# Optimization experiments

Measured on AMD Instinct MI355X. Metric: run time of the kernel, lower is better.

The kernel has to match this reference:

```python
import jax, jax.numpy as jnp
import numpy as np

N_QUBITS = 12
N_LAYERS = 5
OUTPUT_DIM = 4
BATCH = 1024


def _apply_1q(state, U, q, n):
    # state: (B, 2^n) complex; U: (B, 2, 2) per-sample unitary on wire q
    B = state.shape[0]
    s = state.reshape(B, 2 ** q, 2, -1)
    s = jnp.einsum('bik,bakc->baic', U, s)
    return s.reshape(B, -1)


def _cnot(state, c, t, n):
    # CNOT with control wire c, target wire t (wire 0 = most significant bit)
    B = state.shape[0]
    s = state.reshape((B,) + (2,) * n)
    s0 = jax.lax.index_in_dim(s, 0, axis=1 + c, keepdims=True)
    s1 = jax.lax.index_in_dim(s, 1, axis=1 + c, keepdims=True)
    s1 = jnp.flip(s1, axis=1 + t)  # X on target where control = 1
    return jnp.concatenate([s0, s1], axis=1 + c).reshape(B, -1)


def _forward(x, input_weights, theta, output_weights):
    n, L, D = N_QUBITS, N_LAYERS, OUTPUT_DIM
    x = jnp.tanh(x)
    B = x.shape[0]
    # |0...0> initial state, batched
    state = jnp.zeros((B, 2 ** n), jnp.complex64).at[:, 0].set(1.0)
    for l in range(L):
        # data re-uploading: RX(input_weights[l,j] * x[:,j]) on every wire, every layer
        a = input_weights[l][None, :] * x          # (B, n) RX angles
        b = theta[l, :, 0]                          # (n,) RY angles
        c = theta[l, :, 1]                          # (n,) RZ angles
        ca = jnp.cos(a / 2).astype(jnp.complex64)
        sa = jnp.sin(a / 2).astype(jnp.complex64)
        Rx = jnp.stack([jnp.stack([ca, -1j * sa], -1),
                        jnp.stack([-1j * sa, ca], -1)], -2)  # (B, n, 2, 2)
        cb = jnp.cos(b / 2).astype(jnp.complex64)
        sb = jnp.sin(b / 2).astype(jnp.complex64)
        ec = jnp.exp(-1j * c.astype(jnp.complex64) / 2)      # e^{-i c/2}
        # M = RZ(c) @ RY(b), shared across the batch
        M = jnp.stack([jnp.stack([ec * cb, -ec * sb], -1),
                       jnp.stack([jnp.conj(ec) * sb, jnp.conj(ec) * cb], -1)], -2)  # (n,2,2)
        # fused single-qubit unitary U = RZ @ RY @ RX per (sample, wire)
        U = jnp.einsum('qik,bqkj->bqij', M, Rx)
        for q in range(n):
            state = _apply_1q(state, U[:, q], q, n)
        for i in range(n):
            state = _cnot(state, i, (i + 1) % n, n)
    # exact <Z_i> on the first D wires
    p = jnp.abs(state) ** 2  # (B, 2^n)
    zs = []
    for i in range(D):
        pr = p.reshape(B, 2 ** i, 2, -1)
        zs.append(pr[:, :, 0, :].sum((1, 2)) - pr[:, :, 1, :].sum((1, 2)))
    Q = jnp.stack(zs, axis=1)  # (B, D)
    return output_weights[None, :] * Q


def setup_inputs() -> dict:
    key = jax.random.key(0)
    k1, k2, k3, k4 = jax.random.split(key, 4)
    return {
        'x': jax.random.normal(k1, (BATCH, N_QUBITS), jnp.float32),
        'input_weights': jax.random.normal(k2, (N_LAYERS, N_QUBITS), jnp.float32),
        'theta': jax.random.normal(k3, (N_LAYERS, N_QUBITS, 2), jnp.float32),
        'output_weights': jax.random.normal(k4, (OUTPUT_DIM,), jnp.float32),
    }


def reference(x, input_weights, theta, output_weights):
    return _forward(x, input_weights, theta, output_weights)
```

## Files before the change

### kernel.cpp

```cpp
#include <hip/hip_runtime.h>

#define NQ 12
#define NL 5
#define TPB 256

__host__ __device__ constexpr int sfx12_(int x) {
    x ^= x >> 1; x ^= x >> 2; x ^= x >> 4; x ^= x >> 8;
    return x & 0xFFF;
}
__host__ __device__ constexpr int par_(int x) {
    int y = x; y ^= y >> 8; y ^= y >> 4; y ^= y >> 2; y ^= y >> 1;
    return y & 1;
}
__host__ __device__ constexpr int amp_addr(int i) {
    const int g = i >> 1;
    const int G = g ^ ((g >> 3) & 7);
    return (G << 4) | ((i & 1) << 3);
}
__host__ __device__ constexpr int scat_c(int m) {
    const int s = sfx12_(m << 8);
    return amp_addr(s ^ ((s & 1) << 11));
}
__host__ __device__ constexpr int bpat(int m) { return amp_addr(m << 4); }
__host__ __device__ constexpr int meas_h(int m) {
    const int d = sfx12_(m << 8) ^ (par_(m) << 11);
    return (d >> 8) & 15;
}

__device__ __forceinline__ void gate_pair(float2 &a, float2 &c,
        const float2 u00, const float2 u01, const float2 u10, const float2 u11) {
    float2 n0, n1;
    n0.x = fmaf(u00.x, a.x, fmaf(-u00.y, a.y, fmaf(u01.x, c.x, -u01.y * c.y)));
    n0.y = fmaf(u00.x, a.y, fmaf( u00.y, a.x, fmaf(u01.x, c.y,  u01.y * c.x)));
    n1.x = fmaf(u10.x, a.x, fmaf(-u10.y, a.y, fmaf(u11.x, c.x, -u11.y * c.y)));
    n1.y = fmaf(u10.x, a.y, fmaf( u10.y, a.x, fmaf(u11.x, c.y,  u11.y * c.x)));
    a = n0; c = n1;
}
template <int K>
__device__ __forceinline__ void apply_gate(float2 (&v)[16], const float2* __restrict__ Uq) {
    const float2 u00 = Uq[0], u01 = Uq[1], u10 = Uq[2], u11 = Uq[3];
#pragma unroll
    for (int h = 0; h < 8; ++h) {
        const int m0 = ((h >> K) << (K + 1)) | (h & ((1 << K) - 1));
        gate_pair(v[m0], v[m0 | (1 << K)], u00, u01, u10, u11);
    }
}

extern "C" __global__ void __launch_bounds__(TPB)
qnet_kernel(const float* __restrict__ x, const float* __restrict__ iw,
            const float* __restrict__ th, const float* __restrict__ ow,
            float* __restrict__ out) {
    __shared__ float2 st[4096];
    __shared__ __align__(16) float2 U[NL][NQ][4];
    __shared__ float wz[4][4];
    char* stb = (char*)st;

    const int b = blockIdx.x;
    const int tid = threadIdx.x;
    const int w = tid >> 6;

    if (tid < NL * NQ) {
        const int l = tid / NQ, q = tid % NQ;
        const float xv = tanhf(x[b * NQ + q]);
        const float a = iw[l * NQ + q] * xv;
        const float bt = th[(l * NQ + q) * 2 + 0];
        const float ct = th[(l * NQ + q) * 2 + 1];
        float sa, ca; sincosf(0.5f * a, &sa, &ca);
        float sb, cb; sincosf(0.5f * bt, &sb, &cb);
        float sc, cc; sincosf(0.5f * ct, &sc, &cc);
        const float M00r = cc * cb, M00i = -sc * cb;
        const float M01r = -cc * sb, M01i = sc * sb;
        const float M10r = cc * sb, M10i = sc * sb;
        const float M11r = cc * cb, M11i = sc * cb;
        U[l][q][0] = make_float2(fmaf(M00r, ca,  sa * M01i), fmaf(M00i, ca, -sa * M01r));
        U[l][q][1] = make_float2(fmaf(ca, M01r,  sa * M00i), fmaf(ca, M01i, -sa * M00r));
        U[l][q][2] = make_float2(fmaf(M10r, ca,  sa * M11i), fmaf(M10i, ca, -sa * M11r));
        U[l][q][3] = make_float2(fmaf(ca, M11r,  sa * M10i), fmaf(ca, M11i, -sa * M10r));
    }

    const int baseA = amp_addr(tid << 4);
    const int baseB = amp_addr(((tid >> 4) << 8) | (tid & 15));
    const int baseC = amp_addr(tid);
    const int pt = __popc(tid) & 1;
    const int baseS = amp_addr(sfx12_(tid) ^ (pt << 11));
    const int hT = pt << 3;

    __syncthreads();

    float2 v[16];
#pragma unroll 1
    for (int l = 0; l < NL; ++l) {
        if (l == 0) {
#pragma unroll
            for (int r = 0; r < 16; ++r) v[r] = make_float2(0.f, 0.f);
            if (tid == 0) v[0].x = 1.f;
        } else {
#pragma unroll
            for (int c = 0; c < 8; ++c) {
                const float4 f = *(const float4*)(stb + (baseA ^ (c << 4)));
                v[2 * c]     = make_float2(f.x, f.y);
                v[2 * c + 1] = make_float2(f.z, f.w);
            }
        }
        apply_gate<0>(v, U[l][11]);
        apply_gate<1>(v, U[l][10]);
        apply_gate<2>(v, U[l][9]);
        apply_gate<3>(v, U[l][8]);
#pragma unroll
        for (int c = 0; c < 8; ++c)
            *(float4*)(stb + (baseA ^ (c << 4))) =
                make_float4(v[2 * c].x, v[2 * c].y, v[2 * c + 1].x, v[2 * c + 1].y);
        __syncthreads();

#pragma unroll
        for (int m = 0; m < 16; ++m)
            v[m] = *(const float2*)(stb + (baseB ^ bpat(m)));
        apply_gate<0>(v, U[l][7]);
        apply_gate<1>(v, U[l][6]);
        apply_gate<2>(v, U[l][5]);
        apply_gate<3>(v, U[l][4]);
#pragma unroll
        for (int m = 0; m < 16; ++m)
            *(float2*)(stb + (baseB ^ bpat(m))) = v[m];
        __syncthreads();

#pragma unroll
        for (int m = 0; m < 16; ++m)
            v[m] = *(const float2*)(stb + baseC + (m << 11));
        apply_gate<0>(v, U[l][3]);
        apply_gate<1>(v, U[l][2]);
        apply_gate<2>(v, U[l][1]);
        apply_gate<3>(v, U[l][0]);

        if (l != NL - 1) {
            __syncthreads();
#pragma unroll
            for (int m = 0; m < 16; ++m)
                *(float2*)(stb + (baseS ^ scat_c(m))) = v[m];
            __syncthreads();
        }
    }

    float z0 = 0.f, z1 = 0.f, z2 = 0.f, z3 = 0.f;
#pragma unroll
    for (int m = 0; m < 16; ++m) {
        const float pr = fmaf(v[m].x, v[m].x, v[m].y * v[m].y);
        const int h = meas_h(m) ^ hT;
        z0 += (h & 8) ? -pr : pr;
        z1 += (h & 4) ? -pr : pr;
        z2 += (h & 2) ? -pr : pr;
        z3 += (h & 1) ? -pr : pr;
    }
#pragma unroll
    for (int off = 32; off > 0; off >>= 1) {
        z0 += __shfl_xor(z0, off);
        z1 += __shfl_xor(z1, off);
        z2 += __shfl_xor(z2, off);
        z3 += __shfl_xor(z3, off);
    }
    if ((tid & 63) == 0) {
        wz[w][0] = z0; wz[w][1] = z1; wz[w][2] = z2; wz[w][3] = z3;
    }
    __syncthreads();
    if (tid < 4) {
        const float z = wz[0][tid] + wz[1][tid] + wz[2][tid] + wz[3][tid];
        out[b * 4 + tid] = ow[tid] * z;
    }
}

extern "C" void kernel_launch(void* const* d_in, const int* in_sizes, int n_in,
                              void* d_out, int out_size, void* d_ws, size_t ws_size,
                              hipStream_t stream) {
    const float* x  = (const float*)d_in[0];
    const float* iw = (const float*)d_in[1];
    const float* th = (const float*)d_in[2];
    const float* ow = (const float*)d_in[3];
    float* out = (float*)d_out;
    const int batch = in_sizes[0] / NQ;
    hipLaunchKernelGGL(qnet_kernel, dim3(batch), dim3(TPB), 0, stream,
                       x, iw, th, ow, out);
}
```

Before: 50.34 us.

## Use 512 threads with 8 amplitudes each and closed-form first layer

Doubles threads per block to 512, so each thread holds 8 amplitudes instead of 16. Each layer now applies 3 gates per pass over four passes through shared memory instead of 4 gates over three. The first layer is computed in closed form: since the initial state is |0...0>, the state after layer 0 is a product state, permuted by the CNOT ring, and each amplitude is built from products of U entries without touching shared memory. The trade is one extra shared-memory exchange and barrier per layer in return for more parallelism, fewer registers and removal of layer 0's state traffic.

```diff
diff --git a/kernel.cpp b/kernel.cpp
--- a/kernel.cpp
+++ b/kernel.cpp
@@ -2,7 +2,7 @@
 
 #define NQ 12
 #define NL 5
-#define TPB 256
+#define TPB 512
 
 __host__ __device__ constexpr int sfx12_(int x) {
     x ^= x >> 1; x ^= x >> 2; x ^= x >> 4; x ^= x >> 8;
@@ -17,16 +17,16 @@
     const int G = g ^ ((g >> 3) & 7);
     return (G << 4) | ((i & 1) << 3);
 }
-__host__ __device__ constexpr int scat_c(int m) {
-    const int s = sfx12_(m << 8);
-    return amp_addr(s ^ ((s & 1) << 11));
-}
-__host__ __device__ constexpr int bpat(int m) { return amp_addr(m << 4); }
-__host__ __device__ constexpr int meas_h(int m) {
-    const int d = sfx12_(m << 8) ^ (par_(m) << 11);
-    return (d >> 8) & 15;
-}
-
+__host__ __device__ constexpr int fi_(int x) { return sfx12_(x) ^ (par_(x) << 11); }
+__host__ __device__ constexpr int bpatB(int m) { return amp_addr(m << 3); }
+__host__ __device__ constexpr int cpatC(int m) { return amp_addr(m << 6); }
+__host__ __device__ constexpr int dpatD(int m) { return amp_addr(m << 9); }
+__host__ __device__ constexpr int spat9(int m) { return amp_addr(fi_(m << 9)); }
+__host__ __device__ constexpr int mh9(int m)  { return (fi_(m << 9) >> 8) & 15; }
+
+__device__ __forceinline__ float2 cmul(float2 a, float2 b) {
+    return make_float2(fmaf(a.x, b.x, -a.y * b.y), fmaf(a.x, b.y, a.y * b.x));
+}
 __device__ __forceinline__ void gate_pair(float2 &a, float2 &c,
         const float2 u00, const float2 u01, const float2 u10, const float2 u11) {
     float2 n0, n1;
@@ -37,22 +37,22 @@
     a = n0; c = n1;
 }
 template <int K>
-__device__ __forceinline__ void apply_gate(float2 (&v)[16], const float2* __restrict__ Uq) {
+__device__ __forceinline__ void apply_gate8(float2 (&v)[8], const float2* __restrict__ Uq) {
     const float2 u00 = Uq[0], u01 = Uq[1], u10 = Uq[2], u11 = Uq[3];
 #pragma unroll
-    for (int h = 0; h < 8; ++h) {
+    for (int h = 0; h < 4; ++h) {
         const int m0 = ((h >> K) << (K + 1)) | (h & ((1 << K) - 1));
         gate_pair(v[m0], v[m0 | (1 << K)], u00, u01, u10, u11);
     }
 }
 
-extern "C" __global__ void __launch_bounds__(TPB)
+extern "C" __global__ void __launch_bounds__(TPB, 8)
 qnet_kernel(const float* __restrict__ x, const float* __restrict__ iw,
             const float* __restrict__ th, const float* __restrict__ ow,
             float* __restrict__ out) {
     __shared__ float2 st[4096];
     __shared__ __align__(16) float2 U[NL][NQ][4];
-    __shared__ float wz[4][4];
+    __shared__ float wz[8][4];
     char* stb = (char*)st;
 
     const int b = blockIdx.x;
@@ -78,74 +78,107 @@
         U[l][q][3] = make_float2(fmaf(ca, M11r,  sa * M10i), fmaf(ca, M11i, -sa * M10r));
     }
 
-    const int baseA = amp_addr(tid << 4);
-    const int baseB = amp_addr(((tid >> 4) << 8) | (tid & 15));
-    const int baseC = amp_addr(tid);
-    const int pt = __popc(tid) & 1;
-    const int baseS = amp_addr(sfx12_(tid) ^ (pt << 11));
-    const int hT = pt << 3;
+    const int baseA = amp_addr(tid << 3);
+    const int baseB = amp_addr((tid & 7) | ((tid >> 3) << 6));
+    const int baseC = amp_addr((tid & 63) | ((tid >> 6) << 9));
+    const int baseD = amp_addr(tid);
+    const int baseS = amp_addr(fi_(tid));
+    const int hT = (tid >> 8) | ((__popc(tid) & 1) << 3);
 
     __syncthreads();
 
-    float2 v[16];
-#pragma unroll 1
-    for (int l = 0; l < NL; ++l) {
-        if (l == 0) {
-#pragma unroll
-            for (int r = 0; r < 16; ++r) v[r] = make_float2(0.f, 0.f);
-            if (tid == 0) v[0].x = 1.f;
-        } else {
-#pragma unroll
-            for (int c = 0; c < 8; ++c) {
+    float2 v[8];
+    {
+        const int t0 = tid & 1, t1 = (tid >> 1) & 1, t2 = (tid >> 2) & 1;
+        const int t3 = (tid >> 3) & 1, t4 = (tid >> 4) & 1, t5 = (tid >> 5) & 1;
+        const int t6 = (tid >> 6) & 1, t7 = (tid >> 7) & 1, t8 = (tid >> 8) & 1;
+        #define C0(k, bit) (U[0][11 - (k)][(bit) ? 2 : 0])
+        float2 Pm = cmul(C0(3, t0 ^ t1), C0(4, t1 ^ t2));
+        Pm = cmul(Pm, C0(5, t2 ^ t3));
+        Pm = cmul(Pm, C0(6, t3 ^ t4));
+        Pm = cmul(Pm, C0(7, t4 ^ t5));
+        Pm = cmul(Pm, C0(8, t5 ^ t6));
+        Pm = cmul(Pm, C0(9, t6 ^ t7));
+        const float2 H0 = cmul(C0(10, t7 ^ t8),     C0(11, t8));
+        const float2 H1 = cmul(C0(10, t7 ^ t8 ^ 1), C0(11, t8 ^ 1));
+        float2 PH[2];
+        PH[0] = cmul(Pm, H0); PH[1] = cmul(Pm, H1);
+        float2 T[2][2];
+        T[0][0] = cmul(C0(0, 0), PH[0]); T[0][1] = cmul(C0(0, 1), PH[0]);
+        T[1][0] = cmul(C0(0, 1), PH[1]); T[1][1] = cmul(C0(0, 0), PH[1]);
+        const float2 A20 = C0(2, t0), A21 = C0(2, 1 ^ t0);
+        float2 B12[2][2];
+        B12[0][0] = cmul(C0(1, 0), A20); B12[0][1] = cmul(C0(1, 1), A21);
+        B12[1][0] = cmul(C0(1, 1), A20); B12[1][1] = cmul(C0(1, 0), A21);
+        #undef C0
+#pragma unroll
+        for (int r = 0; r < 8; ++r) {
+            const int r0 = r & 1, r1 = (r >> 1) & 1, r2 = (r >> 2) & 1;
+            v[r] = cmul(T[r0][r1], B12[r1][r2]);
+        }
+    }
+
+#pragma unroll
+    for (int l = 1; l < NL; ++l) {
+        if (l > 1) {
+#pragma unroll
+            for (int c = 0; c < 4; ++c) {
                 const float4 f = *(const float4*)(stb + (baseA ^ (c << 4)));
                 v[2 * c]     = make_float2(f.x, f.y);
                 v[2 * c + 1] = make_float2(f.z, f.w);
             }
         }
-        apply_gate<0>(v, U[l][11]);
-        apply_gate<1>(v, U[l][10]);
-        apply_gate<2>(v, U[l][9]);
-        apply_gate<3>(v, U[l][8]);
-#pragma unroll
-        for (int c = 0; c < 8; ++c)
+        apply_gate8<0>(v, U[l][11]);
+        apply_gate8<1>(v, U[l][10]);
+        apply_gate8<2>(v, U[l][9]);
+#pragma unroll
+        for (int c = 0; c < 4; ++c)
             *(float4*)(stb + (baseA ^ (c << 4))) =
                 make_float4(v[2 * c].x, v[2 * c].y, v[2 * c + 1].x, v[2 * c + 1].y);
         __syncthreads();
 
 #pragma unroll
-        for (int m = 0; m < 16; ++m)
-            v[m] = *(const float2*)(stb + (baseB ^ bpat(m)));
-        apply_gate<0>(v, U[l][7]);
-        apply_gate<1>(v, U[l][6]);
-        apply_gate<2>(v, U[l][5]);
-        apply_gate<3>(v, U[l][4]);
-#pragma unroll
-        for (int m = 0; m < 16; ++m)
-            *(float2*)(stb + (baseB ^ bpat(m))) = v[m];
+        for (int m = 0; m < 8; ++m)
+            v[m] = *(const float2*)(stb + (baseB ^ bpatB(m)));
+        apply_gate8<0>(v, U[l][8]);
+        apply_gate8<1>(v, U[l][7]);
+        apply_gate8<2>(v, U[l][6]);
+#pragma unroll
+        for (int m = 0; m < 8; ++m)
+            *(float2*)(stb + (baseB ^ bpatB(m))) = v[m];
         __syncthreads();
 
 #pragma unroll
-        for (int m = 0; m < 16; ++m)
-            v[m] = *(const float2*)(stb + baseC + (m << 11));
-        apply_gate<0>(v, U[l][3]);
-        apply_gate<1>(v, U[l][2]);
-        apply_gate<2>(v, U[l][1]);
-        apply_gate<3>(v, U[l][0]);
-
+        for (int m = 0; m < 8; ++m)
+            v[m] = *(const float2*)(stb + (baseC ^ cpatC(m)));
+        apply_gate8<0>(v, U[l][5]);
+        apply_gate8<1>(v, U[l][4]);
+        apply_gate8<2>(v, U[l][3]);
+#pragma unroll
+        for (int m = 0; m < 8; ++m)
+            *(float2*)(stb + (baseC ^ cpatC(m))) = v[m];
+        __syncthreads();
+
+#pragma unroll
+        for (int m = 0; m < 8; ++m)
+            v[m] = *(const float2*)(stb + (baseD ^ dpatD(m)));
+        apply_gate8<0>(v, U[l][2]);
+        apply_gate8<1>(v, U[l][1]);
+        apply_gate8<2>(v, U[l][0]);
         if (l != NL - 1) {
             __syncthreads();
 #pragma unroll
-            for (int m = 0; m < 16; ++m)
-                *(float2*)(stb + (baseS ^ scat_c(m))) = v[m];
+            for (int m = 0; m < 8; ++m)
+                *(float2*)(stb + (baseS ^ spat9(m))) = v[m];
             __syncthreads();
         }
     }
 
     float z0 = 0.f, z1 = 0.f, z2 = 0.f, z3 = 0.f;
 #pragma unroll
-    for (int m = 0; m < 16; ++m) {
+    for (int m = 0; m < 8; ++m) {
         const float pr = fmaf(v[m].x, v[m].x, v[m].y * v[m].y);
-        const int h = meas_h(m) ^ hT;
+        const int h = mh9(m) ^ hT;
         z0 += (h & 8) ? -pr : pr;
         z1 += (h & 4) ? -pr : pr;
         z2 += (h & 2) ? -pr : pr;
@@ -163,7 +196,9 @@
     }
     __syncthreads();
     if (tid < 4) {
-        const float z = wz[0][tid] + wz[1][tid] + wz[2][tid] + wz[3][tid];
+        float z = 0.f;
+#pragma unroll
+        for (int k = 0; k < 8; ++k) z += wz[k][tid];
         out[b * 4 + tid] = ow[tid] * z;
     }
 }
```

Result: faster. 45.90 us (-8.8%).
